# Kernel optimization log

Measured on AMD Instinct MI355X. Metric: run time of the kernel, lower is better.

Reference implementation:

```python
import jax, jax.numpy as jnp
import numpy as np

BN_EPS = 1e-5


def _bn_relu(x, gamma, beta):
    # training-mode BatchNorm1d over (batch, length) per channel; x: [B,C,N]
    mean = jnp.mean(x, axis=(0, 2), keepdims=True)
    var = jnp.var(x, axis=(0, 2), keepdims=True)  # biased, matching torch normalization
    xh = (x - mean) * jax.lax.rsqrt(var + BN_EPS)
    return jax.nn.relu(xh * gamma[None, :, None] + beta[None, :, None])


def setup_inputs() -> dict:
    key = jax.random.key(0)
    ks = jax.random.split(key, 12)
    B, N, S, C1, C2 = 16, 4096, 1024, 256, 256
    C_in = C1 + C2  # 512
    M0, M1 = 256, 256  # mlp channels
    return {
        "xyz1": jax.random.normal(ks[0], (B, 3, N), dtype=jnp.float32),
        "xyz2": jax.random.normal(ks[1], (B, 3, S), dtype=jnp.float32),
        "points1": jax.random.normal(ks[2], (B, C1, N), dtype=jnp.float32),
        "points2": jax.random.normal(ks[3], (B, C2, S), dtype=jnp.float32),
        "w0": jax.random.normal(ks[4], (M0, C_in), dtype=jnp.float32) * 0.02,
        "b0": jnp.zeros((M0,), dtype=jnp.float32),
        "g0": jnp.ones((M0,), dtype=jnp.float32),
        "be0": jnp.zeros((M0,), dtype=jnp.float32),
        "w1": jax.random.normal(ks[5], (M1, M0), dtype=jnp.float32) * 0.02,
        "b1": jnp.zeros((M1,), dtype=jnp.float32),
        "g1": jnp.ones((M1,), dtype=jnp.float32),
        "be1": jnp.zeros((M1,), dtype=jnp.float32),
    }


def reference(xyz1, xyz2, points1, points2, w0, b0, g0, be0, w1, b1, g1, be1):
    # xyz1: [B,3,N], xyz2: [B,3,S], points1: [B,C1,N], points2: [B,C2,S]
    xyz1_t = xyz1.transpose(0, 2, 1)  # [B,N,3]
    xyz2_t = xyz2.transpose(0, 2, 1)  # [B,S,3]
    p2_t = points2.transpose(0, 2, 1)  # [B,S,C2]

    # squared pairwise distances [B,N,S] via |a|^2 + |b|^2 - 2ab
    d = (jnp.sum(xyz1_t ** 2, -1)[:, :, None]
         + jnp.sum(xyz2_t ** 2, -1)[:, None, :]
         - 2.0 * jnp.einsum('bnd,bsd->bns', xyz1_t, xyz2_t))

    # 3 nearest neighbours (smallest distances)
    neg_d3, idx = jax.lax.top_k(-d, 3)  # [B,N,3]
    dists = -neg_d3

    recip = 1.0 / (dists + 1e-8)
    weight = recip / jnp.sum(recip, axis=-1, keepdims=True)  # [B,N,3]

    gathered = jax.vmap(lambda p, i: p[i])(p2_t, idx)  # [B,N,3,C2]
    interp = jnp.sum(gathered * weight[..., None], axis=2)  # [B,N,C2]

    new_points = jnp.concatenate([points1.transpose(0, 2, 1), interp], axis=-1)  # [B,N,C1+C2]
    x = new_points.transpose(0, 2, 1)  # [B,C_in,N]

    # 1x1 Conv1d == per-position matmul
    x = _bn_relu(jnp.einsum('oi,bin->bon', w0, x) + b0[None, :, None], g0, be0)
    x = _bn_relu(jnp.einsum('oi,bin->bon', w1, x) + b1[None, :, None], g1, be1)
    return x
```

## Files before the change

### kernel.cpp

```cpp
#include <hip/hip_runtime.h>
#include <stdint.h>

using u16 = unsigned short;
using short8 = __attribute__((ext_vector_type(8))) short;
using f32x4  = __attribute__((ext_vector_type(4))) float;
using u32x4  = __attribute__((ext_vector_type(4))) unsigned int;

__device__ __forceinline__ float bf2f(u16 u) {
  return __builtin_bit_cast(float, ((unsigned)u) << 16);
}
__device__ __forceinline__ u16 f2bf(float f) {
  unsigned u = __builtin_bit_cast(unsigned, f);
  u += 0x7FFFu + ((u >> 16) & 1u);
  return (u16)(u >> 16);
}

__device__ __forceinline__ void ins3(float& d0, float& d1, float& d2,
                                     int& i0, int& i1, int& i2, float d, int s) {
  bool c0 = d < d0, c1 = d < d1, c2 = d < d2;
  d2 = c1 ? d1 : (c2 ? d : d2);
  i2 = c1 ? i1 : (c2 ? s : i2);
  d1 = c0 ? d0 : (c1 ? d : d1);
  i1 = c0 ? i0 : (c1 ? s : i1);
  d0 = c0 ? d : d0;
  i0 = c0 ? s : i0;
}

__global__ __launch_bounds__(256, 8) void nn3_kernel(
    const float* __restrict__ xyz1, const float* __restrict__ xyz2,
    int* __restrict__ idx_out, float* __restrict__ w_out) {
  __shared__ __align__(16) float cand[8 * 516];
  const int b = blockIdx.y;
  const int t = threadIdx.x;
  const float* x2 = xyz2 + b * 3072;
  for (int i = t; i < 1024; i += 256) {
    float x = x2[i], y = x2[1024 + i], z = x2[2048 + i];
    f32x4 v = { -2.0f * x, -2.0f * y, -2.0f * z, x*x + y*y + z*z };
    *(f32x4*)&cand[(i >> 7) * 516 + (i & 127) * 4] = v;
  }
  __syncthreads();
  const int q = t >> 3, sub = t & 7;
  const int n = blockIdx.x * 32 + q;
  const float* x1 = xyz1 + b * 12288;
  const float px = x1[n], py = x1[4096 + n], pz = x1[8192 + n];
  float d0 = 1e30f, d1 = 1e30f, d2 = 1e30f;
  int i0 = 0, i1 = 0, i2 = 0;
  const int sbeg = sub << 7;
  const float* reg = &cand[sub * 516];
  #pragma unroll 4
  for (int ii = 0; ii < 128; ++ii) {
    f32x4 c = *(const f32x4*)(reg + ii * 4);
    float d = __builtin_fmaf(px, c[0],
              __builtin_fmaf(py, c[1],
              __builtin_fmaf(pz, c[2], c[3])));
    ins3(d0, d1, d2, i0, i1, i2, d, sbeg + ii);
  }
  for (int st = 1; st <= 4; st <<= 1) {
    float e0 = __shfl_xor(d0, st), e1 = __shfl_xor(d1, st), e2 = __shfl_xor(d2, st);
    int   j0 = __shfl_xor(i0, st), j1 = __shfl_xor(i1, st), j2 = __shfl_xor(i2, st);
    ins3(d0, d1, d2, i0, i1, i2, e0, j0);
    ins3(d0, d1, d2, i0, i1, i2, e1, j1);
    ins3(d0, d1, d2, i0, i1, i2, e2, j2);
  }
  if (sub == 0) {
    const float r1 = px*px + py*py + pz*pz;
    float w0 = 1.0f/(d0 + r1 + 1e-8f), w1 = 1.0f/(d1 + r1 + 1e-8f), w2 = 1.0f/(d2 + r1 + 1e-8f);
    float inv = 1.0f/(w0 + w1 + w2);
    const int pos = b * 4096 + n;
    idx_out[pos*3+0] = i0; idx_out[pos*3+1] = i1; idx_out[pos*3+2] = i2;
    w_out[pos*3+0] = w0*inv; w_out[pos*3+1] = w1*inv; w_out[pos*3+2] = w2*inv;
  }
}

__global__ __launch_bounds__(256) void transpose_cl(
    const float* __restrict__ in, u16* __restrict__ out, int L, int rstride) {
  __shared__ u16 tile[64][66];
  const int b = blockIdx.z;
  in  += (size_t)b * 256 * L;
  out += (size_t)b * L * rstride;
  const int n0 = blockIdx.x * 64, c0 = blockIdx.y * 64;
  const int t = threadIdx.x, ln = t & 63, grp = t >> 6;
  for (int p = 0; p < 16; ++p) {
    int cc = p*4 + grp;
    tile[cc][ln] = f2bf(in[(size_t)(c0 + cc) * L + n0 + ln]);
  }
  __syncthreads();
  for (int p = 0; p < 16; ++p) {
    int nn = p*4 + grp;
    out[(size_t)(n0 + nn) * rstride + c0 + ln] = tile[ln][nn];
  }
}

__global__ __launch_bounds__(256) void cvt_kernel(const float* __restrict__ in,
                                                  u16* __restrict__ out, int n) {
  int i = blockIdx.x * 256 + threadIdx.x;
  if (i < n) out[i] = f2bf(in[i]);
}

__global__ __launch_bounds__(256) void interp_kernel(
    const u16* __restrict__ p2t, const int* __restrict__ idx,
    const float* __restrict__ wgt, u16* __restrict__ A1) {
  const int t = threadIdx.x;
  const int ln = t & 63, grp = t >> 6;
  const int c0 = ln * 4;
  for (int i = 0; i < 16; ++i) {
    const int pos = blockIdx.x * 64 + i * 4 + grp;
    const int b = pos >> 12;
    const int j0 = idx[pos*3+0], j1 = idx[pos*3+1], j2 = idx[pos*3+2];
    const float w0 = wgt[pos*3+0], w1 = wgt[pos*3+1], w2 = wgt[pos*3+2];
    ushort4 v0 = *(const ushort4*)(p2t + ((size_t)(b*1024 + j0)) * 256 + c0);
    ushort4 v1 = *(const ushort4*)(p2t + ((size_t)(b*1024 + j1)) * 256 + c0);
    ushort4 v2 = *(const ushort4*)(p2t + ((size_t)(b*1024 + j2)) * 256 + c0);
    ushort4 o;
    o.x = f2bf(w0*bf2f(v0.x) + w1*bf2f(v1.x) + w2*bf2f(v2.x));
    o.y = f2bf(w0*bf2f(v0.y) + w1*bf2f(v1.y) + w2*bf2f(v2.y));
    o.z = f2bf(w0*bf2f(v0.z) + w1*bf2f(v1.z) + w2*bf2f(v2.z));
    o.w = f2bf(w0*bf2f(v0.w) + w1*bf2f(v1.w) + w2*bf2f(v2.w));
    *(ushort4*)(A1 + (size_t)pos*512 + 256 + c0) = o;
  }
}

__global__ __launch_bounds__(256) void gemm_kernel(
    const u16* __restrict__ A, const u16* __restrict__ Bw,
    const float* __restrict__ bias, u16* __restrict__ Y, int K,
    float* __restrict__ sums, float* __restrict__ sumsq) {
  __shared__ __align__(16) u16 As[128*48];
  __shared__ __align__(16) u16 Bs[128*48];
  const int t = threadIdx.x;
  const int m0 = blockIdx.x * 128, n0 = blockIdx.y * 128;
  const int wave = t >> 6, l = t & 63;
  const int wm = wave & 1, wn = wave >> 1;
  const int lc = l & 15, quad = l >> 4;
  f32x4 acc[4][4] = {};
  const int rowA = t >> 2, kc = (t & 3) * 8;
  for (int k0 = 0; k0 < K; k0 += 32) {
    *(u32x4*)&As[rowA*48 + kc]      = *(const u32x4*)&A[(size_t)(m0 + rowA)*K + k0 + kc];
    *(u32x4*)&As[(rowA+64)*48 + kc] = *(const u32x4*)&A[(size_t)(m0 + rowA + 64)*K + k0 + kc];
    *(u32x4*)&Bs[rowA*48 + kc]      = *(const u32x4*)&Bw[(size_t)(n0 + rowA)*K + k0 + kc];
    *(u32x4*)&Bs[(rowA+64)*48 + kc] = *(const u32x4*)&Bw[(size_t)(n0 + rowA + 64)*K + k0 + kc];
    __syncthreads();
    short8 af[4], bfv[4];
    for (int tm = 0; tm < 4; ++tm)
      af[tm] = *(const short8*)&As[(wm*64 + tm*16 + lc)*48 + quad*8];
    for (int tn = 0; tn < 4; ++tn)
      bfv[tn] = *(const short8*)&Bs[(wn*64 + tn*16 + lc)*48 + quad*8];
    for (int tm = 0; tm < 4; ++tm)
      for (int tn = 0; tn < 4; ++tn)
        acc[tm][tn] = __builtin_amdgcn_mfma_f32_16x16x32_bf16(af[tm], bfv[tn], acc[tm][tn], 0, 0, 0);
    __syncthreads();
  }
  float* sl = (float*)As;
  if (t < 256) sl[t] = 0.0f;
  __syncthreads();
  for (int tn = 0; tn < 4; ++tn) {
    const int colL = wn*64 + tn*16 + lc;
    const float bb = bias[n0 + colL];
    float s = 0.0f, q = 0.0f;
    for (int tm = 0; tm < 4; ++tm) {
      const int row = m0 + wm*64 + tm*16 + quad*4;
      for (int r = 0; r < 4; ++r) {
        float v = acc[tm][tn][r] + bb;
        Y[(size_t)(row + r)*256 + n0 + colL] = f2bf(v);
        s += v; q += v*v;
      }
    }
    s += __shfl_xor(s, 16); s += __shfl_xor(s, 32);
    q += __shfl_xor(q, 16); q += __shfl_xor(q, 32);
    if (quad == 0) {
      atomicAdd(&sl[colL], s);
      atomicAdd(&sl[128 + colL], q);
    }
  }
  __syncthreads();
  if (t < 128) {
    const int bank = (blockIdx.x & 7) * 256;
    atomicAdd(&sums [bank + n0 + t], sl[t]);
    atomicAdd(&sumsq[bank + n0 + t], sl[128 + t]);
  }
}

__global__ void bnprep_kernel(const float* __restrict__ sums, const float* __restrict__ sumsq,
                              const float* __restrict__ g, const float* __restrict__ be,
                              float* __restrict__ scale, float* __restrict__ shift) {
  const int t = threadIdx.x;
  float s = 0.0f, q = 0.0f;
  for (int k = 0; k < 8; ++k) { s += sums[k*256 + t]; q += sumsq[k*256 + t]; }
  const float inv_n = 1.0f / 65536.0f;
  float mean = s * inv_n;
  float var = q * inv_n - mean*mean;
  float a = g[t] * rsqrtf(var + 1e-5f);
  scale[t] = a;
  shift[t] = be[t] - mean * a;
}

__global__ __launch_bounds__(256) void bnrelu_kernel(
    const u16* __restrict__ Y, const float* __restrict__ scale,
    const float* __restrict__ shift, u16* __restrict__ X) {
  const int t = threadIdx.x;
  const int ln = t & 63, grp = t >> 6;
  const int c0 = ln * 4;
  const float a0 = scale[c0], a1 = scale[c0+1], a2 = scale[c0+2], a3 = scale[c0+3];
  const float s0 = shift[c0], s1 = shift[c0+1], s2 = shift[c0+2], s3 = shift[c0+3];
  size_t row0 = (size_t)blockIdx.x * 64;
  for (int it = 0; it < 16; ++it) {
    size_t off = (row0 + it*4 + grp) * 256 + c0;
    ushort4 v = *(const ushort4*)&Y[off];
    float f0 = bf2f(v.x)*a0 + s0, f1 = bf2f(v.y)*a1 + s1;
    float f2v = bf2f(v.z)*a2 + s2, f3 = bf2f(v.w)*a3 + s3;
    ushort4 o;
    o.x = f2bf(f0 > 0.0f ? f0 : 0.0f);
    o.y = f2bf(f1 > 0.0f ? f1 : 0.0f);
    o.z = f2bf(f2v > 0.0f ? f2v : 0.0f);
    o.w = f2bf(f3 > 0.0f ? f3 : 0.0f);
    *(ushort4*)&X[off] = o;
  }
}

__global__ __launch_bounds__(256) void bnrelu_tr_kernel(
    const u16* __restrict__ Y, const float* __restrict__ scale,
    const float* __restrict__ shift, float* __restrict__ out) {
  __shared__ u16 tile[256][66];
  const int t = threadIdx.x;
  const int b = blockIdx.z;
  const int n0 = blockIdx.x * 64;
  const float a = scale[t], s = shift[t];
  for (int nn = 0; nn < 64; ++nn) {
    size_t pos = (size_t)b*4096 + n0 + nn;
    float v = bf2f(Y[pos*256 + t]) * a + s;
    tile[t][nn] = f2bf(v > 0.0f ? v : 0.0f);
  }
  __syncthreads();
  const int ln = t & 63, grp = t >> 6;
  for (int p = 0; p < 64; ++p) {
    int oo = p*4 + grp;
    out[((size_t)b*256 + oo)*4096 + n0 + ln] = bf2f(tile[oo][ln]);
  }
}

extern "C" void kernel_launch(void* const* d_in, const int* in_sizes, int n_in,
                              void* d_out, int out_size, void* d_ws, size_t ws_size,
                              hipStream_t stream) {
  const float* xyz1    = (const float*)d_in[0];
  const float* xyz2    = (const float*)d_in[1];
  const float* points1 = (const float*)d_in[2];
  const float* points2 = (const float*)d_in[3];
  const float* w0      = (const float*)d_in[4];
  const float* b0      = (const float*)d_in[5];
  const float* g0      = (const float*)d_in[6];
  const float* be0     = (const float*)d_in[7];
  const float* w1      = (const float*)d_in[8];
  const float* b1      = (const float*)d_in[9];
  const float* g1      = (const float*)d_in[10];
  const float* be1     = (const float*)d_in[11];
  float* out = (float*)d_out;

  char* ws = (char*)d_ws;
  u16*   A1   = (u16*)ws;
  u16*   X0   = (u16*)ws;
  u16*   Y    = (u16*)(ws + (64ull  << 20));
  u16*   p2t  = (u16*)(ws + (96ull  << 20));
  int*   idxb = (int*)(ws + (104ull << 20));
  float* wgtb = (float*)(ws + (105ull << 20));
  u16*   w0b  = (u16*)(ws + (106ull << 20));
  u16*   w1b  = (u16*)(ws + (106ull << 20) + (256u << 10));
  float* stats= (float*)(ws + (106ull << 20) + (512u << 10));

  float* sums0  = stats;
  float* sumsq0 = stats + 2048;
  float* sums1  = stats + 4096;
  float* sumsq1 = stats + 6144;
  float* scale0 = stats + 8192, *shift0 = stats + 8448;
  float* scale1 = stats + 8704, *shift1 = stats + 8960;

  hipMemsetAsync(stats, 0, 8192 * sizeof(float), stream);
  nn3_kernel<<<dim3(128, 16), 256, 0, stream>>>(xyz1, xyz2, idxb, wgtb);
  transpose_cl<<<dim3(16, 4, 16), 256, 0, stream>>>(points2, p2t, 1024, 256);
  transpose_cl<<<dim3(64, 4, 16), 256, 0, stream>>>(points1, A1, 4096, 512);
  cvt_kernel<<<512, 256, 0, stream>>>(w0, w0b, 131072);
  cvt_kernel<<<256, 256, 0, stream>>>(w1, w1b, 65536);
  interp_kernel<<<1024, 256, 0, stream>>>(p2t, idxb, wgtb, A1);
  gemm_kernel<<<dim3(512, 2), 256, 0, stream>>>(A1, w0b, b0, Y, 512, sums0, sumsq0);
  bnprep_kernel<<<1, 256, 0, stream>>>(sums0, sumsq0, g0, be0, scale0, shift0);
  bnrelu_kernel<<<1024, 256, 0, stream>>>(Y, scale0, shift0, X0);
  gemm_kernel<<<dim3(512, 2), 256, 0, stream>>>(X0, w1b, b1, Y, 256, sums1, sumsq1);
  bnprep_kernel<<<1, 256, 0, stream>>>(sums1, sumsq1, g1, be1, scale1, shift1);
  bnrelu_tr_kernel<<<dim3(64, 1, 16), 256, 0, stream>>>(Y, scale1, shift1, out);
}
```

Before: 310.4 us.

## Fuse first BN+ReLU into second GEMM's A-tile load and widen K tile to 64

Removes the standalone bnrelu kernel by applying the layer-0 scale/shift and ReLU while the second GEMM loads A tiles from global memory. This saves one full read and write of the 65536x256 bf16 intermediate plus a kernel launch. The GEMM K-step is also doubled to 64 with a padded 72-element LDS stride, halving the number of syncs per tile. The cost is extra ALU work in the load path, repeated for each of the two column blocks that read the same A tile.

```diff
diff --git a/kernel.cpp b/kernel.cpp
--- a/kernel.cpp
+++ b/kernel.cpp
@@ -13,6 +13,13 @@
   unsigned u = __builtin_bit_cast(unsigned, f);
   u += 0x7FFFu + ((u >> 16) & 1u);
   return (u16)(u >> 16);
+}
+__device__ __forceinline__ unsigned bn2(unsigned w, float a0, float s0, float a1, float s1) {
+  float f0 = bf2f((u16)(w & 0xFFFFu)) * a0 + s0;
+  float f1 = bf2f((u16)(w >> 16))     * a1 + s1;
+  f0 = f0 > 0.0f ? f0 : 0.0f;
+  f1 = f1 > 0.0f ? f1 : 0.0f;
+  return (unsigned)f2bf(f0) | ((unsigned)f2bf(f1) << 16);
 }
 
 __device__ __forceinline__ void ins3(float& d0, float& d1, float& d2,
@@ -120,33 +127,55 @@
   }
 }
 
+template <int FUSE>
 __global__ __launch_bounds__(256) void gemm_kernel(
     const u16* __restrict__ A, const u16* __restrict__ Bw,
     const float* __restrict__ bias, u16* __restrict__ Y, int K,
-    float* __restrict__ sums, float* __restrict__ sumsq) {
-  __shared__ __align__(16) u16 As[128*48];
-  __shared__ __align__(16) u16 Bs[128*48];
+    float* __restrict__ sums, float* __restrict__ sumsq,
+    const float* __restrict__ bn_scale, const float* __restrict__ bn_shift) {
+  __shared__ __align__(16) u16 As[128*72];
+  __shared__ __align__(16) u16 Bs[128*72];
   const int t = threadIdx.x;
   const int m0 = blockIdx.x * 128, n0 = blockIdx.y * 128;
   const int wave = t >> 6, l = t & 63;
   const int wm = wave & 1, wn = wave >> 1;
   const int lc = l & 15, quad = l >> 4;
   f32x4 acc[4][4] = {};
-  const int rowA = t >> 2, kc = (t & 3) * 8;
-  for (int k0 = 0; k0 < K; k0 += 32) {
-    *(u32x4*)&As[rowA*48 + kc]      = *(const u32x4*)&A[(size_t)(m0 + rowA)*K + k0 + kc];
-    *(u32x4*)&As[(rowA+64)*48 + kc] = *(const u32x4*)&A[(size_t)(m0 + rowA + 64)*K + k0 + kc];
-    *(u32x4*)&Bs[rowA*48 + kc]      = *(const u32x4*)&Bw[(size_t)(n0 + rowA)*K + k0 + kc];
-    *(u32x4*)&Bs[(rowA+64)*48 + kc] = *(const u32x4*)&Bw[(size_t)(n0 + rowA + 64)*K + k0 + kc];
+  const int r = t >> 3, kc = (t & 7) * 8;
+  for (int k0 = 0; k0 < K; k0 += 64) {
+    f32x4 sc_lo, sc_hi, sh_lo, sh_hi;
+    if (FUSE) {
+      sc_lo = *(const f32x4*)&bn_scale[k0 + kc];
+      sc_hi = *(const f32x4*)&bn_scale[k0 + kc + 4];
+      sh_lo = *(const f32x4*)&bn_shift[k0 + kc];
+      sh_hi = *(const f32x4*)&bn_shift[k0 + kc + 4];
+    }
+    #pragma unroll
+    for (int p = 0; p < 4; ++p) {
+      const int row = p*32 + r;
+      u32x4 va = *(const u32x4*)&A [(size_t)(m0 + row)*K + k0 + kc];
+      u32x4 vb = *(const u32x4*)&Bw[(size_t)(n0 + row)*K + k0 + kc];
+      if (FUSE) {
+        va[0] = bn2(va[0], sc_lo[0], sh_lo[0], sc_lo[1], sh_lo[1]);
+        va[1] = bn2(va[1], sc_lo[2], sh_lo[2], sc_lo[3], sh_lo[3]);
+        va[2] = bn2(va[2], sc_hi[0], sh_hi[0], sc_hi[1], sh_hi[1]);
+        va[3] = bn2(va[3], sc_hi[2], sh_hi[2], sc_hi[3], sh_hi[3]);
+      }
+      *(u32x4*)&As[row*72 + kc] = va;
+      *(u32x4*)&Bs[row*72 + kc] = vb;
+    }
     __syncthreads();
-    short8 af[4], bfv[4];
-    for (int tm = 0; tm < 4; ++tm)
-      af[tm] = *(const short8*)&As[(wm*64 + tm*16 + lc)*48 + quad*8];
-    for (int tn = 0; tn < 4; ++tn)
-      bfv[tn] = *(const short8*)&Bs[(wn*64 + tn*16 + lc)*48 + quad*8];
-    for (int tm = 0; tm < 4; ++tm)
+    #pragma unroll
+    for (int h = 0; h < 2; ++h) {
+      short8 af[4], bfv[4];
+      for (int tm = 0; tm < 4; ++tm)
+        af[tm] = *(const short8*)&As[(wm*64 + tm*16 + lc)*72 + h*32 + quad*8];
       for (int tn = 0; tn < 4; ++tn)
-        acc[tm][tn] = __builtin_amdgcn_mfma_f32_16x16x32_bf16(af[tm], bfv[tn], acc[tm][tn], 0, 0, 0);
+        bfv[tn] = *(const short8*)&Bs[(wn*64 + tn*16 + lc)*72 + h*32 + quad*8];
+      for (int tm = 0; tm < 4; ++tm)
+        for (int tn = 0; tn < 4; ++tn)
+          acc[tm][tn] = __builtin_amdgcn_mfma_f32_16x16x32_bf16(af[tm], bfv[tn], acc[tm][tn], 0, 0, 0);
+    }
     __syncthreads();
   }
   float* sl = (float*)As;
@@ -158,9 +187,9 @@
     float s = 0.0f, q = 0.0f;
     for (int tm = 0; tm < 4; ++tm) {
       const int row = m0 + wm*64 + tm*16 + quad*4;
-      for (int r = 0; r < 4; ++r) {
-        float v = acc[tm][tn][r] + bb;
-        Y[(size_t)(row + r)*256 + n0 + colL] = f2bf(v);
+      for (int rr = 0; rr < 4; ++rr) {
+        float v = acc[tm][tn][rr] + bb;
+        Y[(size_t)(row + rr)*256 + n0 + colL] = f2bf(v);
         s += v; q += v*v;
       }
     }
@@ -191,29 +220,6 @@
   float a = g[t] * rsqrtf(var + 1e-5f);
   scale[t] = a;
   shift[t] = be[t] - mean * a;
-}
-
-__global__ __launch_bounds__(256) void bnrelu_kernel(
-    const u16* __restrict__ Y, const float* __restrict__ scale,
-    const float* __restrict__ shift, u16* __restrict__ X) {
-  const int t = threadIdx.x;
-  const int ln = t & 63, grp = t >> 6;
-  const int c0 = ln * 4;
-  const float a0 = scale[c0], a1 = scale[c0+1], a2 = scale[c0+2], a3 = scale[c0+3];
-  const float s0 = shift[c0], s1 = shift[c0+1], s2 = shift[c0+2], s3 = shift[c0+3];
-  size_t row0 = (size_t)blockIdx.x * 64;
-  for (int it = 0; it < 16; ++it) {
-    size_t off = (row0 + it*4 + grp) * 256 + c0;
-    ushort4 v = *(const ushort4*)&Y[off];
-    float f0 = bf2f(v.x)*a0 + s0, f1 = bf2f(v.y)*a1 + s1;
-    float f2v = bf2f(v.z)*a2 + s2, f3 = bf2f(v.w)*a3 + s3;
-    ushort4 o;
-    o.x = f2bf(f0 > 0.0f ? f0 : 0.0f);
-    o.y = f2bf(f1 > 0.0f ? f1 : 0.0f);
-    o.z = f2bf(f2v > 0.0f ? f2v : 0.0f);
-    o.w = f2bf(f3 > 0.0f ? f3 : 0.0f);
-    *(ushort4*)&X[off] = o;
-  }
 }
 
 __global__ __launch_bounds__(256) void bnrelu_tr_kernel(
@@ -256,7 +262,7 @@
 
   char* ws = (char*)d_ws;
   u16*   A1   = (u16*)ws;
-  u16*   X0   = (u16*)ws;
+  u16*   Y2   = (u16*)ws;
   u16*   Y    = (u16*)(ws + (64ull  << 20));
   u16*   p2t  = (u16*)(ws + (96ull  << 20));
   int*   idxb = (int*)(ws + (104ull << 20));
@@ -279,10 +285,9 @@
   cvt_kernel<<<512, 256, 0, stream>>>(w0, w0b, 131072);
   cvt_kernel<<<256, 256, 0, stream>>>(w1, w1b, 65536);
   interp_kernel<<<1024, 256, 0, stream>>>(p2t, idxb, wgtb, A1);
-  gemm_kernel<<<dim3(512, 2), 256, 0, stream>>>(A1, w0b, b0, Y, 512, sums0, sumsq0);
+  gemm_kernel<0><<<dim3(512, 2), 256, 0, stream>>>(A1, w0b, b0, Y, 512, sums0, sumsq0, nullptr, nullptr);
   bnprep_kernel<<<1, 256, 0, stream>>>(sums0, sumsq0, g0, be0, scale0, shift0);
-  bnrelu_kernel<<<1024, 256, 0, stream>>>(Y, scale0, shift0, X0);
-  gemm_kernel<<<dim3(512, 2), 256, 0, stream>>>(X0, w1b, b1, Y, 256, sums1, sumsq1);
+  gemm_kernel<1><<<dim3(512, 2), 256, 0, stream>>>(Y, w1b, b1, Y2, 256, sums1, sumsq1, scale0, shift0);
   bnprep_kernel<<<1, 256, 0, stream>>>(sums1, sumsq1, g1, be1, scale1, shift1);
-  bnrelu_tr_kernel<<<dim3(64, 1, 16), 256, 0, stream>>>(Y, scale1, shift1, out);
-}
+  bnrelu_tr_kernel<<<dim3(64, 1, 16), 256, 0, stream>>>(Y2, scale1, shift1, out);
+}
```

Measured after the change: 295.7 us. 1.05x faster.
